# Optimization experiments

Hardware: AMD Instinct MI355X
Metric: run time of the kernel (lower is better)

Reference implementation:

```python
import jax, jax.numpy as jnp
import numpy as np

N = 100000      # nodes
E = 1600000     # edges (avg degree 16)
DIN, DH, DOUT = 128, 128, 64


def setup_inputs() -> dict:
    key = jax.random.key(0)
    k0, k1, k2, k3 = jax.random.split(key, 4)
    x = jax.random.normal(k0, (N, DIN), jnp.float32)
    edge_index = jax.random.randint(k1, (2, E), 0, N, dtype=jnp.int64)
    W1 = jax.random.normal(k2, (DIN, DH), jnp.float32) / np.sqrt(DIN).astype(np.float32)
    b1 = jnp.zeros((DH,), jnp.float32)
    W2 = jax.random.normal(k3, (DH, DOUT), jnp.float32) / np.sqrt(DH).astype(np.float32)
    b2 = jnp.zeros((DOUT,), jnp.float32)
    return {"x": x, "edge_index": edge_index, "W1": W1, "b1": b1, "W2": W2, "b2": b2}


def reference(x, edge_index, W1, b1, W2, b2):
    n = x.shape[0]
    # PyG GCNConv: add self-loops, symmetric normalization deg^-1/2 A_hat deg^-1/2
    loops = jnp.arange(n, dtype=edge_index.dtype)
    src = jnp.concatenate([edge_index[0], loops])  # message sources
    dst = jnp.concatenate([edge_index[1], loops])  # aggregation targets
    deg = jax.ops.segment_sum(jnp.ones(src.shape, x.dtype), dst, num_segments=n)
    dinv = jnp.where(deg > 0, jax.lax.rsqrt(deg), 0.0)
    norm = dinv[src] * dinv[dst]                    # [E+N]

    def gcn_conv(h, W, b):
        h = h @ W                                   # dense transform first (PyG order)
        msg = h[src] * norm[:, None]                # gather + scale
        return jax.ops.segment_sum(msg, dst, num_segments=n) + b

    h = jax.nn.relu(gcn_conv(x, W1, b1))
    # F.dropout is identity in eval mode (self.training == False)
    return gcn_conv(h, W2, b2)
```

## Files before the change

kernel.cpp:

```cpp
#include <hip/hip_runtime.h>

#define DIN 128
#define DH  128
#define DOUT 64

typedef __attribute__((ext_vector_type(8))) short bf16x8;
typedef __attribute__((ext_vector_type(4))) float f32x4;


__device__ inline unsigned bf16rne(float f) {
    unsigned u = __float_as_uint(f);
    return (u + 0x7fffu + ((u >> 16) & 1u)) >> 16;
}

__device__ inline void acc8(float* a, uint4 v) {
    a[0] += __uint_as_float(v.x << 16); a[1] += __uint_as_float(v.x & 0xffff0000u);
    a[2] += __uint_as_float(v.y << 16); a[3] += __uint_as_float(v.y & 0xffff0000u);
    a[4] += __uint_as_float(v.z << 16); a[5] += __uint_as_float(v.z & 0xffff0000u);
    a[6] += __uint_as_float(v.w << 16); a[7] += __uint_as_float(v.w & 0xffff0000u);
}


__global__ void k_count_rank(const int* __restrict__ dst, int* __restrict__ cnt,
                             int* __restrict__ rank, int E, int pad) {
    int e = blockIdx.x * 256 + threadIdx.x;
    if (e < E) rank[e] = atomicAdd(&cnt[dst[e] * pad], 1);
}

__global__ void k_dinv(const int* __restrict__ cnt, float* __restrict__ dinv, int n, int pad) {
    int i = blockIdx.x * 256 + threadIdx.x;
    if (i < n) dinv[i] = rsqrtf((float)(cnt[i * pad] + 1));
}

__global__ void k_scan_partial(const int* __restrict__ cnt, int* __restrict__ excl,
                               int* __restrict__ bsum, int n, int pad) {
    __shared__ int sd[256];
    int t = threadIdx.x;
    int base = blockIdx.x * 1024 + t * 4;
    int v0 = (base + 0 < n) ? cnt[(base + 0) * pad] : 0;
    int v1 = (base + 1 < n) ? cnt[(base + 1) * pad] : 0;
    int v2 = (base + 2 < n) ? cnt[(base + 2) * pad] : 0;
    int v3 = (base + 3 < n) ? cnt[(base + 3) * pad] : 0;
    int s = v0 + v1 + v2 + v3;
    sd[t] = s;
    __syncthreads();
    for (int off = 1; off < 256; off <<= 1) {
        int x = (t >= off) ? sd[t - off] : 0;
        __syncthreads();
        sd[t] += x;
        __syncthreads();
    }
    int incl = sd[t];
    if (t == 255) bsum[blockIdx.x] = incl;
    int run = incl - s;
    if (base + 0 < n) excl[base + 0] = run;  run += v0;
    if (base + 1 < n) excl[base + 1] = run;  run += v1;
    if (base + 2 < n) excl[base + 2] = run;  run += v2;
    if (base + 3 < n) excl[base + 3] = run;
}

__global__ void k_scan_bsum(int* __restrict__ bsum, int nb) {
    __shared__ int sd[256];
    int t = threadIdx.x;
    int v = (t < nb) ? bsum[t] : 0;
    sd[t] = v;
    __syncthreads();
    for (int off = 1; off < 256; off <<= 1) {
        int x = (t >= off) ? sd[t - off] : 0;
        __syncthreads();
        sd[t] += x;
        __syncthreads();
    }
    if (t < nb) bsum[t] = sd[t] - v;
}

__global__ void k_finalize(int* __restrict__ rowstart, const int* __restrict__ bsum,
                           int n, int E) {
    int i = blockIdx.x * 256 + threadIdx.x;
    if (i < n) rowstart[i] += bsum[i >> 10];
    if (i == 0) rowstart[n] = E;
}

__global__ void k_fill2(const int* __restrict__ src, const int* __restrict__ dst,
                        const int* __restrict__ rank, const int* __restrict__ rowstart,
                        int* __restrict__ adj, int E) {
    int e = blockIdx.x * 256 + threadIdx.x;
    if (e < E) adj[rowstart[dst[e]] + rank[e]] = src[e];
}


__global__ void k_wsplit_frag(const float* __restrict__ W, unsigned short* __restrict__ Wf_hi,
                              unsigned short* __restrict__ Wf_lo, int N) {
    int idx = blockIdx.x * 256 + threadIdx.x;
    if (idx >= N * 128) return;
    int f = idx >> 9;
    int r = idx & 511;
    int lane = r >> 3;
    int j = r & 7;
    int t = f >> 2;
    int ks = f & 3;
    int n = t * 16 + (lane & 15);
    int k = ks * 32 + (lane >> 4) * 8 + j;
    float v = W[(size_t)k * N + n];
    unsigned h = bf16rne(v);
    float hf = __uint_as_float(h << 16);
    unsigned l = bf16rne(v - hf);
    Wf_hi[idx] = (unsigned short)h;
    Wf_lo[idx] = (unsigned short)l;
}


template <int NCOLS>
__global__ __launch_bounds__(256, 4) void k_gemm_mfma(
        const float* __restrict__ A,
        const unsigned short* __restrict__ Bh,
        const unsigned short* __restrict__ Bl,
        const float* __restrict__ dinv,
        unsigned short* __restrict__ S, int M) {
    constexpr int NT = NCOLS / 16;
    int wave = threadIdx.x >> 6;
    int lane = threadIdx.x & 63;
    int row0 = blockIdx.x * 64 + wave * 16;
    int arow = row0 + (lane & 15);
    if (arow >= M) arow = M - 1;
    const float* ap = A + (size_t)arow * 128 + (lane >> 4) * 8;
    const unsigned short* bhp = Bh + lane * 8;
    const unsigned short* blp = Bl + lane * 8;

    float4 a0 = *(const float4*)(ap);
    float4 a1 = *(const float4*)(ap + 4);

    f32x4 acc[NT];
    #pragma unroll
    for (int t = 0; t < NT; t++) acc[t] = (f32x4){0.f, 0.f, 0.f, 0.f};

    #pragma unroll
    for (int ks = 0; ks < 4; ks++) {
        float4 n0, n1;
        if (ks < 3) {
            n0 = *(const float4*)(ap + (ks + 1) * 32);
            n1 = *(const float4*)(ap + (ks + 1) * 32 + 4);
        }
        float a8[8] = {a0.x, a0.y, a0.z, a0.w, a1.x, a1.y, a1.z, a1.w};
        bf16x8 ahi, alo;
        #pragma unroll
        for (int j = 0; j < 8; j++) {
            unsigned h = bf16rne(a8[j]);
            float hf = __uint_as_float(h << 16);
            ahi[j] = (short)h;
            alo[j] = (short)bf16rne(a8[j] - hf);
        }
        #pragma unroll
        for (int t = 0; t < NT; t++) {
            bf16x8 bh = *(const bf16x8*)(bhp + (size_t)(t * 4 + ks) * 512);
            bf16x8 bl = *(const bf16x8*)(blp + (size_t)(t * 4 + ks) * 512);
            acc[t] = __builtin_amdgcn_mfma_f32_16x16x32_bf16(ahi, bh, acc[t], 0, 0, 0);
            acc[t] = __builtin_amdgcn_mfma_f32_16x16x32_bf16(ahi, bl, acc[t], 0, 0, 0);
            acc[t] = __builtin_amdgcn_mfma_f32_16x16x32_bf16(alo, bh, acc[t], 0, 0, 0);
        }
        a0 = n0; a1 = n1;
    }

    int srow0 = row0 + (lane >> 4) * 4;
    int bcol = lane & 15;
    #pragma unroll
    for (int r = 0; r < 4; r++) {
        int row = srow0 + r;
        float dv = (row < M) ? dinv[row] : 0.f;
        #pragma unroll
        for (int t = 0; t < NT; t++) {
            unsigned o = bf16rne(dv * acc[t][r]);
            unsigned p = (unsigned)__shfl_xor((int)o, 1);
            if ((lane & 1) == 0 && row < M)
                *(unsigned*)(S + (size_t)row * NCOLS + t * 16 + bcol) = o | (p << 16);
        }
    }
}


template <bool RELU>
__global__ void k_agg128(const unsigned short* __restrict__ S, const int* __restrict__ rowstart,
                         const int* __restrict__ adj, const float* __restrict__ dinv,
                         const float* __restrict__ bias, float* __restrict__ out, int n) {
    int wave = threadIdx.x >> 6;
    int lane = threadIdx.x & 63;
    int node = blockIdx.x * 4 + wave;
    if (node >= n) return;
    int start = rowstart[node];
    int end   = rowstart[node + 1];
    int g  = lane >> 4;
    int fo = lane & 15;

    const uint4* S4 = (const uint4*)S;
    float a0[8] = {}, a1[8] = {};

    while (start < end) {
        int cnt = end - start;
        if (cnt > 64) cnt = 64;
        int nb = adj[start + (lane < cnt ? lane : cnt - 1)];
        int t = 0;
        for (; t + 16 <= cnt; t += 16) {
            int jA = __shfl(nb, t + 0  + g);
            int jB = __shfl(nb, t + 4  + g);
            int jC = __shfl(nb, t + 8  + g);
            int jD = __shfl(nb, t + 12 + g);
            uint4 mA = S4[(size_t)jA * 16 + fo];
            uint4 mB = S4[(size_t)jB * 16 + fo];
            uint4 mC = S4[(size_t)jC * 16 + fo];
            uint4 mD = S4[(size_t)jD * 16 + fo];
            acc8(a0, mA); acc8(a1, mB); acc8(a0, mC); acc8(a1, mD);
        }
        for (; t + 4 <= cnt; t += 4) {
            int j = __shfl(nb, t + g);
            uint4 m = S4[(size_t)j * 16 + fo];
            acc8(a0, m);
        }
        if (t < cnt) {
            int i1 = t + g;
            int j = __shfl(nb, i1 < cnt ? i1 : cnt - 1);
            uint4 m = S4[(size_t)j * 16 + fo];
            if (i1 < cnt) acc8(a1, m);
        }
        start += 64;
    }

    float acc[8];
    #pragma unroll
    for (int i = 0; i < 8; i++) {
        float v = a0[i] + a1[i];
        v += __shfl_xor(v, 16);
        v += __shfl_xor(v, 32);
        acc[i] = v;
    }

    uint4 selfu = ((const uint4*)S)[(size_t)node * 16 + fo];
    float self[8] = {};
    acc8(self, selfu);
    float dv = dinv[node];
    float4 bb0 = ((const float4*)bias)[fo * 2 + 0];
    float4 bb1 = ((const float4*)bias)[fo * 2 + 1];
    float o[8];
    o[0] = dv * (acc[0] + self[0]) + bb0.x;
    o[1] = dv * (acc[1] + self[1]) + bb0.y;
    o[2] = dv * (acc[2] + self[2]) + bb0.z;
    o[3] = dv * (acc[3] + self[3]) + bb0.w;
    o[4] = dv * (acc[4] + self[4]) + bb1.x;
    o[5] = dv * (acc[5] + self[5]) + bb1.y;
    o[6] = dv * (acc[6] + self[6]) + bb1.z;
    o[7] = dv * (acc[7] + self[7]) + bb1.w;
    if (RELU) {
        #pragma unroll
        for (int i = 0; i < 8; i++) o[i] = fmaxf(o[i], 0.f);
    }
    if (g == 0) {
        float4* op = (float4*)(out + (size_t)node * 128 + fo * 8);
        op[0] = make_float4(o[0], o[1], o[2], o[3]);
        op[1] = make_float4(o[4], o[5], o[6], o[7]);
    }
}

__global__ void k_agg64(const unsigned short* __restrict__ S, const int* __restrict__ rowstart,
                        const int* __restrict__ adj, const float* __restrict__ dinv,
                        const float* __restrict__ bias, float* __restrict__ out, int n) {
    int wave = threadIdx.x >> 6;
    int lane = threadIdx.x & 63;
    int node = blockIdx.x * 4 + wave;
    if (node >= n) return;
    int start = rowstart[node];
    int end   = rowstart[node + 1];
    int g  = lane >> 3;
    int fo = lane & 7;

    const uint4* S4 = (const uint4*)S;
    float a0[8] = {}, a1[8] = {};

    while (start < end) {
        int cnt = end - start;
        if (cnt > 64) cnt = 64;
        int nb = adj[start + (lane < cnt ? lane : cnt - 1)];
        int t = 0;
        for (; t + 32 <= cnt; t += 32) {
            int jA = __shfl(nb, t + 0  + g);
            int jB = __shfl(nb, t + 8  + g);
            int jC = __shfl(nb, t + 16 + g);
            int jD = __shfl(nb, t + 24 + g);
            uint4 mA = S4[(size_t)jA * 8 + fo];
            uint4 mB = S4[(size_t)jB * 8 + fo];
            uint4 mC = S4[(size_t)jC * 8 + fo];
            uint4 mD = S4[(size_t)jD * 8 + fo];
            acc8(a0, mA); acc8(a1, mB); acc8(a0, mC); acc8(a1, mD);
        }
        for (; t + 8 <= cnt; t += 8) {
            int j = __shfl(nb, t + g);
            uint4 m = S4[(size_t)j * 8 + fo];
            acc8(a0, m);
        }
        if (t < cnt) {
            int i1 = t + g;
            int j = __shfl(nb, i1 < cnt ? i1 : cnt - 1);
            uint4 m = S4[(size_t)j * 8 + fo];
            if (i1 < cnt) acc8(a1, m);
        }
        start += 64;
    }

    float acc[8];
    #pragma unroll
    for (int i = 0; i < 8; i++) {
        float v = a0[i] + a1[i];
        v += __shfl_xor(v, 8);
        v += __shfl_xor(v, 16);
        v += __shfl_xor(v, 32);
        acc[i] = v;
    }

    uint4 selfu = ((const uint4*)S)[(size_t)node * 8 + fo];
    float self[8] = {};
    acc8(self, selfu);
    float dv = dinv[node];
    float4 bb0 = ((const float4*)bias)[fo * 2 + 0];
    float4 bb1 = ((const float4*)bias)[fo * 2 + 1];
    float o[8];
    o[0] = dv * (acc[0] + self[0]) + bb0.x;
    o[1] = dv * (acc[1] + self[1]) + bb0.y;
    o[2] = dv * (acc[2] + self[2]) + bb0.z;
    o[3] = dv * (acc[3] + self[3]) + bb0.w;
    o[4] = dv * (acc[4] + self[4]) + bb1.x;
    o[5] = dv * (acc[5] + self[5]) + bb1.y;
    o[6] = dv * (acc[6] + self[6]) + bb1.z;
    o[7] = dv * (acc[7] + self[7]) + bb1.w;
    if (g == 0) {
        float4* op = (float4*)(out + (size_t)node * 64 + fo * 8);
        op[0] = make_float4(o[0], o[1], o[2], o[3]);
        op[1] = make_float4(o[4], o[5], o[6], o[7]);
    }
}


extern "C" void kernel_launch(void* const* d_in, const int* in_sizes, int n_in,
                              void* d_out, int out_size, void* d_ws, size_t ws_size,
                              hipStream_t stream) {
    const float* x  = (const float*)d_in[0];
    const int*   ei = (const int*)d_in[1];
    const float* W1 = (const float*)d_in[2];
    const float* b1 = (const float*)d_in[3];
    const float* W2 = (const float*)d_in[4];
    const float* b2 = (const float*)d_in[5];
    float* out = (float*)d_out;

    int N = in_sizes[0] / DIN;
    int E = in_sizes[1] / 2;
    const int* esrc = ei;
    const int* edst = ei + E;

    size_t fixed = (size_t)N * 128 * 2
                 + (size_t)N * 128 * 4
                 + (size_t)N * 4
                 + (size_t)(N + 1) * 4
                 + (size_t)E * 4 * 2
                 + (128 + 64) * 128 * 2 * 2
                 + 1024 * 4 + 16 * 256;
    int PAD = (fixed + (size_t)N * 16 * 4 <= ws_size) ? 16 : 1;

    char* wsb = (char*)d_ws;
    size_t off = 0;
    auto alloc = [&](size_t bytes) {
        void* p = wsb + off;
        off = (off + bytes + 255) & ~(size_t)255;
        return p;
    };
    unsigned short* S = (unsigned short*)alloc((size_t)N * 128 * 2);
    float* H1       = (float*)alloc((size_t)N * 128 * 4);
    float* dinv     = (float*)alloc((size_t)N * 4);
    int*   rowstart = (int*)alloc((size_t)(N + 1) * 4);
    int*   adj      = (int*)alloc((size_t)E * 4);
    int*   rank     = (int*)alloc((size_t)E * 4);
    unsigned short* wf1h = (unsigned short*)alloc(128 * 128 * 2);
    unsigned short* wf1l = (unsigned short*)alloc(128 * 128 * 2);
    unsigned short* wf2h = (unsigned short*)alloc(64 * 128 * 2);
    unsigned short* wf2l = (unsigned short*)alloc(64 * 128 * 2);
    int*   cnt      = (int*)alloc((size_t)N * PAD * 4);
    int*   bsum     = (int*)alloc(1024 * 4);

    int eb = (E + 255) / 256;
    int nb = (N + 255) / 256;
    int sb = (N + 1023) / 1024;

    k_wsplit_frag<<<(128 * 128) / 256, 256, 0, stream>>>(W1, wf1h, wf1l, 128);
    k_wsplit_frag<<<(64 * 128) / 256, 256, 0, stream>>>(W2, wf2h, wf2l, 64);

    hipMemsetAsync(cnt, 0, (size_t)N * PAD * 4, stream);
    k_count_rank<<<eb, 256, 0, stream>>>(edst, cnt, rank, E, PAD);
    k_dinv<<<nb, 256, 0, stream>>>(cnt, dinv, N, PAD);
    k_scan_partial<<<sb, 256, 0, stream>>>(cnt, rowstart, bsum, N, PAD);
    k_scan_bsum<<<1, 256, 0, stream>>>(bsum, sb);
    k_finalize<<<nb, 256, 0, stream>>>(rowstart, bsum, N, E);
    k_fill2<<<eb, 256, 0, stream>>>(esrc, edst, rank, rowstart, adj, E);

    int gb = (N + 63) / 64;
    int ab = (N + 3) / 4;

    k_gemm_mfma<128><<<gb, 256, 0, stream>>>(x, wf1h, wf1l, dinv, S, N);
    k_agg128<true><<<ab, 256, 0, stream>>>(S, rowstart, adj, dinv, b1, H1, N);

    k_gemm_mfma<64><<<gb, 256, 0, stream>>>(H1, wf2h, wf2l, dinv, S, N);
    k_agg64<<<ab, 256, 0, stream>>>(S, rowstart, adj, dinv, b2, out, N);
}
```

Baseline: 268.5 us.

## Store layer-1 activations as bf16 and co-launch adjacency fill with first GEMM

The first aggregation now writes H1 as bf16 instead of fp32, which halves the intermediate traffic. A new GEMM variant reads bf16 A directly, dropping the hi/lo split of the activation operand so only the weights keep two terms. Separately, the CSR fill kernel is merged into the first GEMM launch as extra blocks so the two independent jobs can overlap and one launch goes away. The trade-off is lower precision in the second-layer input, since H1 is rounded to bf16.

```diff
diff --git a/kernel.cpp b/kernel.cpp
--- a/kernel.cpp
+++ b/kernel.cpp
@@ -79,13 +79,6 @@
     int i = blockIdx.x * 256 + threadIdx.x;
     if (i < n) rowstart[i] += bsum[i >> 10];
     if (i == 0) rowstart[n] = E;
-}
-
-__global__ void k_fill2(const int* __restrict__ src, const int* __restrict__ dst,
-                        const int* __restrict__ rank, const int* __restrict__ rowstart,
-                        int* __restrict__ adj, int E) {
-    int e = blockIdx.x * 256 + threadIdx.x;
-    if (e < E) adj[rowstart[dst[e]] + rank[e]] = src[e];
 }
 
 
@@ -111,16 +104,14 @@
 
 
 template <int NCOLS>
-__global__ __launch_bounds__(256, 4) void k_gemm_mfma(
-        const float* __restrict__ A,
-        const unsigned short* __restrict__ Bh,
-        const unsigned short* __restrict__ Bl,
-        const float* __restrict__ dinv,
-        unsigned short* __restrict__ S, int M) {
+__device__ __forceinline__ void gemm_f32A_body(
+        int bid, const float* __restrict__ A,
+        const unsigned short* __restrict__ Bh, const unsigned short* __restrict__ Bl,
+        const float* __restrict__ dinv, unsigned short* __restrict__ S, int M) {
     constexpr int NT = NCOLS / 16;
     int wave = threadIdx.x >> 6;
     int lane = threadIdx.x & 63;
-    int row0 = blockIdx.x * 64 + wave * 16;
+    int row0 = bid * 64 + wave * 16;
     int arow = row0 + (lane & 15);
     if (arow >= M) arow = M - 1;
     const float* ap = A + (size_t)arow * 128 + (lane >> 4) * 8;
@@ -177,11 +168,78 @@
     }
 }
 
-
-template <bool RELU>
+template <int NCOLS>
+__global__ __launch_bounds__(256, 4) void k_fill_gemm(
+        const int* __restrict__ src, const int* __restrict__ dst,
+        const int* __restrict__ rank, const int* __restrict__ rowstart,
+        int* __restrict__ adj, int E, int gemm_blocks,
+        const float* __restrict__ A, const unsigned short* __restrict__ Bh,
+        const unsigned short* __restrict__ Bl, const float* __restrict__ dinv,
+        unsigned short* __restrict__ S, int M) {
+    int bid = blockIdx.x;
+    if (bid < gemm_blocks) {
+        gemm_f32A_body<NCOLS>(bid, A, Bh, Bl, dinv, S, M);
+    } else {
+        int e = (bid - gemm_blocks) * 256 + threadIdx.x;
+        if (e < E) adj[rowstart[dst[e]] + rank[e]] = src[e];
+    }
+}
+
+template <int NCOLS>
+__global__ __launch_bounds__(256, 4) void k_gemm_bf16A(
+        const unsigned short* __restrict__ A,
+        const unsigned short* __restrict__ Bh, const unsigned short* __restrict__ Bl,
+        const float* __restrict__ dinv, unsigned short* __restrict__ S, int M) {
+    constexpr int NT = NCOLS / 16;
+    int wave = threadIdx.x >> 6;
+    int lane = threadIdx.x & 63;
+    int row0 = blockIdx.x * 64 + wave * 16;
+    int arow = row0 + (lane & 15);
+    if (arow >= M) arow = M - 1;
+    const unsigned short* ap = A + (size_t)arow * 128 + (lane >> 4) * 8;
+    const unsigned short* bhp = Bh + lane * 8;
+    const unsigned short* blp = Bl + lane * 8;
+
+    bf16x8 a = *(const bf16x8*)(ap);
+
+    f32x4 acc[NT];
+    #pragma unroll
+    for (int t = 0; t < NT; t++) acc[t] = (f32x4){0.f, 0.f, 0.f, 0.f};
+
+    #pragma unroll
+    for (int ks = 0; ks < 4; ks++) {
+        bf16x8 anext;
+        if (ks < 3) anext = *(const bf16x8*)(ap + (ks + 1) * 32);
+        #pragma unroll
+        for (int t = 0; t < NT; t++) {
+            bf16x8 bh = *(const bf16x8*)(bhp + (size_t)(t * 4 + ks) * 512);
+            bf16x8 bl = *(const bf16x8*)(blp + (size_t)(t * 4 + ks) * 512);
+            acc[t] = __builtin_amdgcn_mfma_f32_16x16x32_bf16(a, bh, acc[t], 0, 0, 0);
+            acc[t] = __builtin_amdgcn_mfma_f32_16x16x32_bf16(a, bl, acc[t], 0, 0, 0);
+        }
+        a = anext;
+    }
+
+    int srow0 = row0 + (lane >> 4) * 4;
+    int bcol = lane & 15;
+    #pragma unroll
+    for (int r = 0; r < 4; r++) {
+        int row = srow0 + r;
+        float dv = (row < M) ? dinv[row] : 0.f;
+        #pragma unroll
+        for (int t = 0; t < NT; t++) {
+            unsigned o = bf16rne(dv * acc[t][r]);
+            unsigned p = (unsigned)__shfl_xor((int)o, 1);
+            if ((lane & 1) == 0 && row < M)
+                *(unsigned*)(S + (size_t)row * NCOLS + t * 16 + bcol) = o | (p << 16);
+        }
+    }
+}
+
+
 __global__ void k_agg128(const unsigned short* __restrict__ S, const int* __restrict__ rowstart,
                          const int* __restrict__ adj, const float* __restrict__ dinv,
-                         const float* __restrict__ bias, float* __restrict__ out, int n) {
+                         const float* __restrict__ bias, unsigned short* __restrict__ out, int n) {
     int wave = threadIdx.x >> 6;
     int lane = threadIdx.x & 63;
     int node = blockIdx.x * 4 + wave;
@@ -248,14 +306,15 @@
     o[5] = dv * (acc[5] + self[5]) + bb1.y;
     o[6] = dv * (acc[6] + self[6]) + bb1.z;
     o[7] = dv * (acc[7] + self[7]) + bb1.w;
-    if (RELU) {
-        #pragma unroll
-        for (int i = 0; i < 8; i++) o[i] = fmaxf(o[i], 0.f);
-    }
+    #pragma unroll
+    for (int i = 0; i < 8; i++) o[i] = fmaxf(o[i], 0.f);
     if (g == 0) {
-        float4* op = (float4*)(out + (size_t)node * 128 + fo * 8);
-        op[0] = make_float4(o[0], o[1], o[2], o[3]);
-        op[1] = make_float4(o[4], o[5], o[6], o[7]);
+        uint4 w;
+        w.x = bf16rne(o[0]) | (bf16rne(o[1]) << 16);
+        w.y = bf16rne(o[2]) | (bf16rne(o[3]) << 16);
+        w.z = bf16rne(o[4]) | (bf16rne(o[5]) << 16);
+        w.w = bf16rne(o[6]) | (bf16rne(o[7]) << 16);
+        ((uint4*)out)[(size_t)node * 16 + fo] = w;
     }
 }
 
@@ -354,7 +413,7 @@
     const int* edst = ei + E;
 
     size_t fixed = (size_t)N * 128 * 2
-                 + (size_t)N * 128 * 4
+                 + (size_t)N * 128 * 2
                  + (size_t)N * 4
                  + (size_t)(N + 1) * 4
                  + (size_t)E * 4 * 2
@@ -369,8 +428,8 @@
         off = (off + bytes + 255) & ~(size_t)255;
         return p;
     };
-    unsigned short* S = (unsigned short*)alloc((size_t)N * 128 * 2);
-    float* H1       = (float*)alloc((size_t)N * 128 * 4);
+    unsigned short* S  = (unsigned short*)alloc((size_t)N * 128 * 2);
+    unsigned short* H1 = (unsigned short*)alloc((size_t)N * 128 * 2);
     float* dinv     = (float*)alloc((size_t)N * 4);
     int*   rowstart = (int*)alloc((size_t)(N + 1) * 4);
     int*   adj      = (int*)alloc((size_t)E * 4);
@@ -395,14 +454,14 @@
     k_scan_partial<<<sb, 256, 0, stream>>>(cnt, rowstart, bsum, N, PAD);
     k_scan_bsum<<<1, 256, 0, stream>>>(bsum, sb);
     k_finalize<<<nb, 256, 0, stream>>>(rowstart, bsum, N, E);
-    k_fill2<<<eb, 256, 0, stream>>>(esrc, edst, rank, rowstart, adj, E);
 
     int gb = (N + 63) / 64;
     int ab = (N + 3) / 4;
 
-    k_gemm_mfma<128><<<gb, 256, 0, stream>>>(x, wf1h, wf1l, dinv, S, N);
-    k_agg128<true><<<ab, 256, 0, stream>>>(S, rowstart, adj, dinv, b1, H1, N);
-
-    k_gemm_mfma<64><<<gb, 256, 0, stream>>>(H1, wf2h, wf2l, dinv, S, N);
+    k_fill_gemm<128><<<gb + eb, 256, 0, stream>>>(esrc, edst, rank, rowstart, adj, E, gb,
+                                                  x, wf1h, wf1l, dinv, S, N);
+    k_agg128<<<ab, 256, 0, stream>>>(S, rowstart, adj, dinv, b1, H1, N);
+
+    k_gemm_bf16A<64><<<gb, 256, 0, stream>>>(H1, wf2h, wf2l, dinv, S, N);
     k_agg64<<<ab, 256, 0, stream>>>(S, rowstart, adj, dinv, b2, out, N);
 }
```

New measurement: 250.5 us (median of 3 runs). 6.7% less time.
